# Kernel tuning notes

Measured on AMD Instinct MI355X. Metric: run time of the kernel, lower is better.

## Reference

```python
import jax, jax.numpy as jnp
import numpy as np

D_MODEL = 1024
N_HEADS = 16
D_Q = 64
D_V = 64
N_SEG = 16
EPS_LN = 1e-5
EPS_MEM = 1e-6


def setup_inputs() -> dict:
    key = jax.random.key(0)
    ks = jax.random.split(key, 10)
    N, T = 4, 4096
    inp = {
        "query_sequences": jax.random.normal(ks[0], (N, T, D_MODEL), dtype=jnp.float32),
        "key_sequences": jax.random.normal(ks[1], (N, T, D_MODEL), dtype=jnp.float32),
        "value_sequences": jax.random.normal(ks[2], (N, T, D_MODEL), dtype=jnp.float32),
        "Wq": jax.random.normal(ks[3], (D_MODEL, N_HEADS * D_Q), dtype=jnp.float32) * 0.02,
        "Wk": jax.random.normal(ks[4], (D_MODEL, N_HEADS * D_Q), dtype=jnp.float32) * 0.02,
        "Wv": jax.random.normal(ks[5], (D_MODEL, N_HEADS * D_V), dtype=jnp.float32) * 0.02,
        "Wo": jax.random.normal(ks[6], (N_HEADS * D_V, D_MODEL), dtype=jnp.float32) * 0.02,
        "ln_w": jnp.ones((D_MODEL,), dtype=jnp.float32),
        "ln_b": jnp.zeros((D_MODEL,), dtype=jnp.float32),
        "beta": jnp.ones((1,), dtype=jnp.float32),
    }
    return inp


def _layer_norm(x, w, b):
    mu = jnp.mean(x, axis=-1, keepdims=True)
    var = jnp.var(x, axis=-1, keepdims=True)
    return (x - mu) * jax.lax.rsqrt(var + EPS_LN) * w + b


def reference(query_sequences, key_sequences, value_sequences, Wq, Wk, Wv, Wo, ln_w, ln_b, beta):
    N, t, _ = query_sequences.shape
    S = t // N_SEG  # segment length (256)

    # qkv_norm applied to q, and (self-attention) to k and v as well
    qn = _layer_norm(query_sequences, ln_w, ln_b)
    kn = _layer_norm(key_sequences, ln_w, ln_b)
    vn = _layer_norm(value_sequences, ln_w, ln_b)

    # project and split heads -> [N, H, t, d]
    qh = (qn @ Wq).reshape(N, t, N_HEADS, D_Q).transpose(0, 2, 1, 3)
    kh = (kn @ Wk).reshape(N, t, N_HEADS, D_Q).transpose(0, 2, 1, 3)
    vh = (vn @ Wv).reshape(N, t, N_HEADS, D_V).transpose(0, 2, 1, 3)

    # segment: [N_SEG, N, H, S, d] so lax.scan iterates segments sequentially
    seg = lambda x, d: x.reshape(N, N_HEADS, N_SEG, S, d).transpose(2, 0, 1, 3, 4)
    q_segs, k_segs, v_segs = seg(qh, D_Q), seg(kh, D_Q), seg(vh, D_V)

    b_gate = jax.nn.sigmoid(beta)[0]            # scalar mixing gate
    scale = 1.0 / np.sqrt(D_Q).astype(np.float32)
    causal = jnp.tril(jnp.ones((S, S), dtype=bool))

    def step(carry, xs):
        mem, z = carry                          # [N,H,Dq,Dv], [N,H,Dq]
        qs, ks_, vs = xs                        # [N,H,S,d]
        sq = jax.nn.elu(qs) + 1.0
        sk = jax.nn.elu(ks_) + 1.0
        # retrieve from compressive memory
        num = jnp.einsum('nhsd,nhde->nhse', sq, mem)
        den = jnp.einsum('nhsd,nhd->nhs', sq, z)[..., None] + EPS_MEM
        a_mem = num / den                       # [N,H,S,Dv]
        # local causal softmax attention within the segment
        scores = jnp.einsum('nhsd,nhtd->nhst', qs, ks_) * scale
        scores = jnp.where(causal, scores, -jnp.inf)
        probs = jax.nn.softmax(scores, axis=-1)
        attn = jnp.einsum('nhst,nhtd->nhsd', probs, vs)
        out = b_gate * a_mem + (1.0 - b_gate) * attn
        # linear memory update
        mem = mem + jnp.einsum('nhsd,nhse->nhde', sk, vs)
        z = z + sk.sum(axis=2)
        return (mem, z), out

    mem0 = jnp.zeros((N, N_HEADS, D_Q, D_V), dtype=query_sequences.dtype)
    z0 = jnp.zeros((N, N_HEADS, D_Q), dtype=query_sequences.dtype)
    _, outs = jax.lax.scan(step, (mem0, z0), (q_segs, k_segs, v_segs))

    # outs: [N_SEG, N, H, S, Dv] -> [N, t, H*Dv]
    seqs = outs.transpose(1, 0, 3, 2, 4).reshape(N, t, N_HEADS * D_V)
    return seqs @ Wo
```

## Files before the change

kernel.cpp:

```cpp
#include <hip/hip_runtime.h>
#include <stdint.h>
#include <math.h>


typedef __attribute__((ext_vector_type(8))) short bf16x8_t;
typedef __attribute__((ext_vector_type(4))) short short4_t;
typedef __attribute__((ext_vector_type(4))) float f32x4;

__device__ __forceinline__ float bf2f(short s){
  union { unsigned u; float f; } v; v.u = ((unsigned)(unsigned short)s) << 16; return v.f;
}
__device__ __forceinline__ short f2bf(float f){
  union { float fl; unsigned u; } v; v.fl = f;
  unsigned r = v.u + 0x7FFFu + ((v.u >> 16) & 1u);
  return (short)(unsigned short)(r >> 16);
}
__device__ __forceinline__ f32x4 mfma16(bf16x8_t a, bf16x8_t b, f32x4 c){
  return __builtin_amdgcn_mfma_f32_16x16x32_bf16(a, b, c, 0, 0, 0);
}
__device__ __forceinline__ void gl_lds16(const short* g, short* l){
  __builtin_amdgcn_global_load_lds((const __attribute__((address_space(1))) void*)g,
                                   (__attribute__((address_space(3))) void*)l, 16, 0, 0);
}

__global__ __launch_bounds__(256) void ln_kernel(const float* __restrict__ x,
                                                 const float* __restrict__ gw,
                                                 const float* __restrict__ gb,
                                                 short* __restrict__ out){
  const int row = blockIdx.x, tid = threadIdx.x;
  const float4 v = *reinterpret_cast<const float4*>(x + (size_t)row*1024 + tid*4);
  float s  = v.x + v.y + v.z + v.w;
  float s2 = v.x*v.x + v.y*v.y + v.z*v.z + v.w*v.w;
  #pragma unroll
  for (int off = 1; off < 64; off <<= 1){
    s  += __shfl_xor(s,  off);
    s2 += __shfl_xor(s2, off);
  }
  __shared__ float red[8];
  if ((tid & 63) == 0){ red[tid>>6] = s; red[4 + (tid>>6)] = s2; }
  __syncthreads();
  s  = red[0] + red[1] + red[2] + red[3];
  s2 = red[4] + red[5] + red[6] + red[7];
  const float mu  = s * (1.0f/1024.0f);
  const float var = s2 * (1.0f/1024.0f) - mu*mu;
  const float rs  = rsqrtf(var + 1e-5f);
  const float4 wv = *reinterpret_cast<const float4*>(gw + tid*4);
  const float4 bv = *reinterpret_cast<const float4*>(gb + tid*4);
  short4_t o;
  o[0] = f2bf((v.x-mu)*rs*wv.x + bv.x);
  o[1] = f2bf((v.y-mu)*rs*wv.y + bv.y);
  o[2] = f2bf((v.z-mu)*rs*wv.z + bv.z);
  o[3] = f2bf((v.w-mu)*rs*wv.w + bv.w);
  *reinterpret_cast<short4_t*>(out + (size_t)row*1024 + tid*4) = o;
}

__global__ __launch_bounds__(256) void wcast(const float* __restrict__ W, short* __restrict__ Wt){
  __shared__ float tile[64][65];
  const int bx = blockIdx.x, by = blockIdx.y, tid = threadIdx.x;
  #pragma unroll
  for (int p=0;p<4;++p){
    int idx = p*256 + tid;
    int r = idx >> 4, c4 = (idx & 15) << 2;
    const float4 v = *reinterpret_cast<const float4*>(W + (size_t)(by*64 + r)*1024 + bx*64 + c4);
    tile[r][c4+0] = v.x; tile[r][c4+1] = v.y; tile[r][c4+2] = v.z; tile[r][c4+3] = v.w;
  }
  __syncthreads();
  #pragma unroll
  for (int p=0;p<4;++p){
    int idx = p*256 + tid;
    int r = idx >> 4, c4 = (idx & 15) << 2;
    short4_t o;
    o[0] = f2bf(tile[c4+0][r]); o[1] = f2bf(tile[c4+1][r]);
    o[2] = f2bf(tile[c4+2][r]); o[3] = f2bf(tile[c4+3][r]);
    *reinterpret_cast<short4_t*>(Wt + (size_t)(bx*64 + r)*1024 + by*64 + c4) = o;
  }
}

__global__ __launch_bounds__(512, 2) void gemm256(const short* __restrict__ A, const short* __restrict__ Bt,
                                                  void* __restrict__ C, int mode){
  extern __shared__ short smem[];
  short* As = smem;
  short* Bs = smem + 32768;
  const int tid = threadIdx.x;
  const int m0 = blockIdx.x * 256;
  const int c0 = blockIdx.y * 256;
  const int lane = tid & 63, wid = tid >> 6;
  const int wr = wid >> 2, wc = wid & 3;
  const int l15 = lane & 15, lhi = lane >> 4;

  const short* Asrc[4]; const short* Bsrc[4];
  #pragma unroll
  for (int p=0;p<4;++p){
    int i = tid + 512*p;
    int r = i >> 3, g = (i & 7) ^ (r & 7);
    Asrc[p] = A  + (size_t)(m0 + r)*1024 + g*8;
    Bsrc[p] = Bt + (size_t)(c0 + r)*1024 + g*8;
  }

  f32x4 acc[8][4];
  #pragma unroll
  for (int m=0;m<8;++m)
    #pragma unroll
    for (int n=0;n<4;++n) acc[m][n] = (f32x4){0.f,0.f,0.f,0.f};

  #define STAGE_A(t) { short* _d=&As[((t)&1)<<14]; int _k=(t)<<6; \
      gl_lds16(Asrc[0]+_k, _d+tid*8); gl_lds16(Asrc[1]+_k, _d+4096+tid*8); \
      gl_lds16(Asrc[2]+_k, _d+8192+tid*8); gl_lds16(Asrc[3]+_k, _d+12288+tid*8); }
  #define STAGE_B(t) { short* _d=&Bs[((t)&1)<<14]; int _k=(t)<<6; \
      gl_lds16(Bsrc[0]+_k, _d+tid*8); gl_lds16(Bsrc[1]+_k, _d+4096+tid*8); \
      gl_lds16(Bsrc[2]+_k, _d+8192+tid*8); gl_lds16(Bsrc[3]+_k, _d+12288+tid*8); }

  STAGE_A(0); STAGE_B(0);
  asm volatile("s_waitcnt vmcnt(0)" ::: "memory");
  __builtin_amdgcn_s_barrier();

  for (int t = 0; t < 16; ++t){
    const short* Ab = &As[(t & 1) << 14];
    const short* Bb = &Bs[(t & 1) << 14];
    if (t < 15){ STAGE_A(t+1); STAGE_B(t+1); }
    bf16x8_t af[4][2], bfr[4][2];
    #pragma unroll
    for (int m=0;m<4;++m){
      int r = wr*128 + m*16 + l15;
      #pragma unroll
      for (int ks=0;ks<2;++ks){
        int sl = (ks*4 + lhi) ^ (r & 7);
        af[m][ks] = *reinterpret_cast<const bf16x8_t*>(&Ab[r*64 + sl*8]);
      }
    }
    #pragma unroll
    for (int n=0;n<2;++n){
      int r = wc*64 + n*16 + l15;
      #pragma unroll
      for (int ks=0;ks<2;++ks){
        int sl = (ks*4 + lhi) ^ (r & 7);
        bfr[n][ks] = *reinterpret_cast<const bf16x8_t*>(&Bb[r*64 + sl*8]);
      }
    }
    __builtin_amdgcn_s_setprio(1);
    #pragma unroll
    for (int m=0;m<4;++m)
      #pragma unroll
      for (int n=0;n<2;++n)
        #pragma unroll
        for (int ks=0;ks<2;++ks)
          acc[m][n] = mfma16(af[m][ks], bfr[n][ks], acc[m][n]);
    __builtin_amdgcn_s_setprio(0);
    #pragma unroll
    for (int n=2;n<4;++n){
      int r = wc*64 + n*16 + l15;
      #pragma unroll
      for (int ks=0;ks<2;++ks){
        int sl = (ks*4 + lhi) ^ (r & 7);
        bfr[n][ks] = *reinterpret_cast<const bf16x8_t*>(&Bb[r*64 + sl*8]);
      }
    }
    __builtin_amdgcn_s_setprio(1);
    #pragma unroll
    for (int m=0;m<4;++m)
      #pragma unroll
      for (int n=2;n<4;++n)
        #pragma unroll
        for (int ks=0;ks<2;++ks)
          acc[m][n] = mfma16(af[m][ks], bfr[n][ks], acc[m][n]);
    __builtin_amdgcn_s_setprio(0);
    #pragma unroll
    for (int m=0;m<4;++m){
      int r = wr*128 + 64 + m*16 + l15;
      #pragma unroll
      for (int ks=0;ks<2;++ks){
        int sl = (ks*4 + lhi) ^ (r & 7);
        af[m][ks] = *reinterpret_cast<const bf16x8_t*>(&Ab[r*64 + sl*8]);
      }
    }
    __builtin_amdgcn_s_setprio(1);
    #pragma unroll
    for (int m=0;m<4;++m)
      #pragma unroll
      for (int n=0;n<2;++n)
        #pragma unroll
        for (int ks=0;ks<2;++ks)
          acc[4+m][n] = mfma16(af[m][ks], bfr[n][ks], acc[4+m][n]);
    __builtin_amdgcn_s_setprio(0);
    __builtin_amdgcn_s_setprio(1);
    #pragma unroll
    for (int m=0;m<4;++m)
      #pragma unroll
      for (int n=2;n<4;++n)
        #pragma unroll
        for (int ks=0;ks<2;++ks)
          acc[4+m][n] = mfma16(af[m][ks], bfr[n][ks], acc[4+m][n]);
    __builtin_amdgcn_s_setprio(0);
    asm volatile("s_waitcnt vmcnt(0)" ::: "memory");
    __builtin_amdgcn_s_barrier();
  }
  #undef STAGE_A
  #undef STAGE_B

  if (mode == 0){
    short* Cb = (short*)C;
    #pragma unroll
    for (int m=0;m<8;++m)
      #pragma unroll
      for (int n=0;n<4;++n)
        #pragma unroll
        for (int j=0;j<4;++j){
          int row = m0 + wr*128 + m*16 + lhi*4 + j;
          int col = c0 + wc*64 + n*16 + l15;
          size_t oidx = ((size_t)((row>>12)*16 + (col>>6)) * 4096 + (size_t)(row & 4095)) * 64 + (col & 63);
          Cb[oidx] = f2bf(acc[m][n][j]);
        }
  } else if (mode == 2){
    short* Cb = (short*)C;
    #pragma unroll
    for (int m=0;m<8;++m)
      #pragma unroll
      for (int n=0;n<4;++n){
        int rowb = m0 + wr*128 + m*16 + lhi*4;
        int col  = c0 + wc*64 + n*16 + l15;
        int nh = ((rowb>>12)<<4) + (col>>6);
        int e  = col & 63;
        int tt = rowb & 4095;
        short4_t o;
        #pragma unroll
        for (int j=0;j<4;++j) o[j] = f2bf(acc[m][n][j]);
        *reinterpret_cast<short4_t*>(&Cb[((size_t)nh*64 + e)*4096 + tt]) = o;
      }
  } else {
    float* Cf = (float*)C;
    #pragma unroll
    for (int m=0;m<8;++m)
      #pragma unroll
      for (int n=0;n<4;++n)
        #pragma unroll
        for (int j=0;j<4;++j){
          int row = m0 + wr*128 + m*16 + lhi*4 + j;
          int col = c0 + wc*64 + n*16 + l15;
          Cf[(size_t)row*1024 + col] = acc[m][n][j];
        }
  }
}

__global__ __launch_bounds__(256) void stageA(const short* __restrict__ kh, const short* __restrict__ vhT,
                                              short* __restrict__ delta_b, float* __restrict__ zd){
  const int seg = blockIdx.x, nh = blockIdx.y, tid = threadIdx.x;
  const int lane = tid & 63, w = tid >> 6;
  const int l15 = lane & 15, lhi = lane >> 4;
  __shared__ short skT[64*256];
  const size_t thead = (size_t)nh*4096 + (size_t)seg*256;

  #pragma unroll
  for (int ch=0; ch<8; ++ch){
    int s  = ch*32 + (tid>>3);
    int lc = (tid&7)*8;
    bf16x8_t kv = *reinterpret_cast<const bf16x8_t*>(kh + (thead + s)*64 + lc);
    #pragma unroll
    for (int j=0;j<8;++j){
      float f = bf2f(kv[j]);
      short sv = f2bf((f > 0.f) ? (f + 1.f) : __expf(f));
      int d = lc + j;
      int bo = ((d*256 + s) << 1) ^ (((d>>3)&7) << 4);
      *reinterpret_cast<short*>(reinterpret_cast<char*>(skT) + bo) = sv;
    }
  }
  __syncthreads();

  bf16x8_t ones;
  #pragma unroll
  for (int i=0;i<8;++i) ones[i] = (short)0x3F80;

  f32x4 dacc[4], zacc[4];
  #pragma unroll
  for (int jf=0;jf<4;++jf){ dacc[jf] = (f32x4){0.f,0.f,0.f,0.f}; zacc[jf] = (f32x4){0.f,0.f,0.f,0.f}; }

  #pragma unroll
  for (int ks=0; ks<8; ++ks){
    bf16x8_t av = *reinterpret_cast<const bf16x8_t*>(
        vhT + ((size_t)nh*64 + w*16 + l15)*4096 + (size_t)seg*256 + ks*32 + lhi*8);
    #pragma unroll
    for (int jf=0;jf<4;++jf){
      int d  = jf*16 + l15;
      int so = ks*32 + lhi*8;
      int bo = ((d*256 + so) << 1) ^ (((d>>3)&7) << 4);
      bf16x8_t bk = *reinterpret_cast<const bf16x8_t*>(reinterpret_cast<char*>(skT) + bo);
      dacc[jf] = mfma16(av, bk, dacc[jf]);
      if (w == 0) zacc[jf] = mfma16(ones, bk, zacc[jf]);
    }
  }

  short* dp = delta_b + (size_t)(seg*64 + nh)*4096;
  #pragma unroll
  for (int jf=0;jf<4;++jf)
    #pragma unroll
    for (int j=0;j<4;++j)
      dp[(w*16 + lhi*4 + j)*64 + jf*16 + l15] = f2bf(dacc[jf][j]);
  if (w == 0 && lhi == 0){
    #pragma unroll
    for (int jf=0;jf<4;++jf)
      zd[(size_t)(seg*64 + nh)*64 + jf*16 + l15] = zacc[jf][0];
  }
}

__global__ __launch_bounds__(256) void stageB(const short* __restrict__ delta_b, const float* __restrict__ zd,
                                              short* __restrict__ mpre_b, float* __restrict__ zpre){
  const int c = blockIdx.x, nh = blockIdx.y, tid = threadIdx.x;
  const int idx = c*256 + tid;
  float acc = 0.f;
  for (int seg=0; seg<16; ++seg){
    size_t b = (size_t)(seg*64 + nh)*4096 + idx;
    mpre_b[b] = f2bf(acc);
    acc += bf2f(delta_b[b]);
  }
  if (c == 0 && tid < 64){
    float za = 0.f;
    for (int seg=0; seg<16; ++seg){
      size_t zb = (size_t)(seg*64 + nh)*64 + tid;
      zpre[zb] = za;
      za += zd[zb];
    }
  }
}

__global__ __launch_bounds__(256, 3) void stageC(const short* __restrict__ qh, const short* __restrict__ kh,
    const short* __restrict__ vhT, const short* __restrict__ mpre_b, const float* __restrict__ z_pre,
    const float* __restrict__ beta, short* __restrict__ seqs)
{
  const int half = blockIdx.x;
  const int seg  = blockIdx.y;
  const int nh   = blockIdx.z;
  const int tid = threadIdx.x;
  const int lane = tid & 63, w = tid >> 6;
  const int l15 = lane & 15, lhi = lane >> 4;

  __shared__ float zl[64];
  __shared__ short pl[4][32][72];

  const size_t thead = (size_t)nh*4096 + (size_t)seg*256;

  if (tid < 64) zl[tid] = z_pre[(size_t)(seg*64 + nh)*64 + tid];
  __syncthreads();

  const float bg = 1.f / (1.f + __expf(-beta[0]));
  const float scale = 0.125f;
  bf16x8_t ones;
  #pragma unroll
  for (int i=0;i<8;++i) ones[i] = (short)0x3F80;

  const int tile = 2*w + (half ? (1 - (w & 1)) : (w & 1));
  const int nkt  = (tile >> 1) + 1;
  const int rb   = tile * 32;

  bf16x8_t aq[2][2];
  #pragma unroll
  for (int m=0;m<2;++m)
    #pragma unroll
    for (int ks=0;ks<2;++ks)
      aq[m][ks] = *reinterpret_cast<const bf16x8_t*>(qh + (thead + rb + m*16 + l15)*64 + ks*32 + lhi*8);

  f32x4 o_acc[2][4], l_acc[2];
  #pragma unroll
  for (int m=0;m<2;++m){
    l_acc[m] = (f32x4){0.f,0.f,0.f,0.f};
    #pragma unroll
    for (int jf=0;jf<4;++jf) o_acc[m][jf] = (f32x4){0.f,0.f,0.f,0.f};
  }

  for (int kt = 0; kt < nkt; ++kt){
    f32x4 s_acc[2][4];
    #pragma unroll
    for (int m=0;m<2;++m)
      #pragma unroll
      for (int jf=0;jf<4;++jf) s_acc[m][jf] = (f32x4){0.f,0.f,0.f,0.f};
    #pragma unroll
    for (int ks=0;ks<2;++ks){
      bf16x8_t bk[4];
      #pragma unroll
      for (int jf=0;jf<4;++jf)
        bk[jf] = *reinterpret_cast<const bf16x8_t*>(kh + (thead + kt*64 + jf*16 + l15)*64 + ks*32 + lhi*8);
      #pragma unroll
      for (int m=0;m<2;++m)
        #pragma unroll
        for (int jf=0;jf<4;++jf)
          s_acc[m][jf] = mfma16(aq[m][ks], bk[jf], s_acc[m][jf]);
    }
    const bool lastkt = (kt == nkt - 1);
    #pragma unroll
    for (int m=0;m<2;++m)
      #pragma unroll
      for (int jf=0;jf<4;++jf)
        #pragma unroll
        for (int j=0;j<4;++j){
          float vv = s_acc[m][jf][j] * scale;
          if (lastkt){
            int sr = rb + m*16 + lhi*4 + j;
            int tc = kt*64 + jf*16 + l15;
            if (tc > sr) vv = -INFINITY;
          }
          float pv = __expf(vv);
          pl[w][m*16 + lhi*4 + j][jf*16 + l15] = f2bf(pv);
        }
    #pragma unroll
    for (int ks2=0;ks2<2;++ks2){
      bf16x8_t ap[2], bv[4];
      #pragma unroll
      for (int m=0;m<2;++m)
        ap[m] = *reinterpret_cast<const bf16x8_t*>(&pl[w][m*16 + l15][ks2*32 + lhi*8]);
      #pragma unroll
      for (int jf=0;jf<4;++jf)
        bv[jf] = *reinterpret_cast<const bf16x8_t*>(
            vhT + ((size_t)nh*64 + jf*16 + l15)*4096 + (size_t)seg*256 + kt*64 + ks2*32 + lhi*8);
      #pragma unroll
      for (int m=0;m<2;++m){
        l_acc[m] = mfma16(ap[m], ones, l_acc[m]);
        #pragma unroll
        for (int jf=0;jf<4;++jf)
          o_acc[m][jf] = mfma16(ap[m], bv[jf], o_acc[m][jf]);
      }
    }
  }

  bf16x8_t sq[2][2];
  #pragma unroll
  for (int m=0;m<2;++m)
    #pragma unroll
    for (int ks=0;ks<2;++ks)
      #pragma unroll
      for (int i=0;i<8;++i){
        float f = bf2f(aq[m][ks][i]);
        sq[m][ks][i] = f2bf((f > 0.f) ? (f + 1.f) : __expf(f));
      }
  bf16x8_t bz[2];
  #pragma unroll
  for (int ks=0;ks<2;++ks)
    #pragma unroll
    for (int i=0;i<8;++i) bz[ks][i] = f2bf(zl[ks*32 + lhi*8 + i]);

  const short* mpbase = mpre_b + (size_t)(seg*64 + nh)*4096;
  f32x4 n_acc[2][4], d_acc[2];
  #pragma unroll
  for (int m=0;m<2;++m){
    d_acc[m] = (f32x4){0.f,0.f,0.f,0.f};
    #pragma unroll
    for (int jf=0;jf<4;++jf) n_acc[m][jf] = (f32x4){0.f,0.f,0.f,0.f};
  }
  #pragma unroll
  for (int ks=0;ks<2;++ks){
    bf16x8_t bm[4];
    #pragma unroll
    for (int jf=0;jf<4;++jf)
      bm[jf] = *reinterpret_cast<const bf16x8_t*>(mpbase + (jf*16 + l15)*64 + ks*32 + lhi*8);
    #pragma unroll
    for (int m=0;m<2;++m){
      #pragma unroll
      for (int jf=0;jf<4;++jf) n_acc[m][jf] = mfma16(sq[m][ks], bm[jf], n_acc[m][jf]);
      d_acc[m] = mfma16(sq[m][ks], bz[ks], d_acc[m]);
    }
  }

  const int nb = nh >> 4, hh = nh & 15;
  #pragma unroll
  for (int m=0;m<2;++m)
    #pragma unroll
    for (int jf=0;jf<4;++jf)
      #pragma unroll
      for (int j=0;j<4;++j){
        float attn = o_acc[m][jf][j] / l_acc[m][j];
        float amem = n_acc[m][jf][j] / (d_acc[m][j] + 1e-6f);
        float ov = bg*amem + (1.f-bg)*attn;
        int srow = rb + m*16 + lhi*4 + j;
        seqs[((size_t)nb*4096 + (size_t)seg*256 + srow)*1024 + hh*64 + jf*16 + l15] = f2bf(ov);
      }
}

extern "C" void kernel_launch(void* const* d_in, const int* in_sizes, int n_in,
                              void* d_out, int out_size, void* d_ws, size_t ws_size,
                              hipStream_t stream){
  (void)in_sizes; (void)n_in; (void)out_size; (void)ws_size;
  const float* q    = (const float*)d_in[0];
  const float* k    = (const float*)d_in[1];
  const float* v    = (const float*)d_in[2];
  const float* Wq   = (const float*)d_in[3];
  const float* Wk   = (const float*)d_in[4];
  const float* Wv   = (const float*)d_in[5];
  const float* Wo   = (const float*)d_in[6];
  const float* lnw  = (const float*)d_in[7];
  const float* lnb  = (const float*)d_in[8];
  const float* beta = (const float*)d_in[9];
  char* ws = (char*)d_ws;
  const size_t MB = 1024ull*1024ull;
  short* WqT    = (short*)(ws + 0*MB);
  short* WkT    = (short*)(ws + 2*MB);
  short* WvT    = (short*)(ws + 4*MB);
  short* WoT    = (short*)(ws + 6*MB);
  short* xn     = (short*)(ws + 8*MB);
  short* seqs   = xn;
  short* qh     = (short*)(ws + 40*MB);
  short* kh     = (short*)(ws + 72*MB);
  short* vhT    = (short*)(ws + 104*MB);
  short* delta_b= (short*)(ws + 136*MB);
  float* zd     = (float*)(ws + 144*MB);
  short* mpre_b = (short*)(ws + 145*MB);
  float* zpre   = (float*)(ws + 153*MB);

  dim3 tg(16,16);
  wcast<<<tg,256,0,stream>>>(Wq, WqT);
  wcast<<<tg,256,0,stream>>>(Wk, WkT);
  wcast<<<tg,256,0,stream>>>(Wv, WvT);
  wcast<<<tg,256,0,stream>>>(Wo, WoT);

  dim3 gg(64,4);
  const size_t lds_gemm = 131072;
  ln_kernel<<<16384,256,0,stream>>>(q, lnw, lnb, xn);
  gemm256<<<gg,512,lds_gemm,stream>>>(xn, WqT, (void*)qh, 0);
  ln_kernel<<<16384,256,0,stream>>>(k, lnw, lnb, xn);
  gemm256<<<gg,512,lds_gemm,stream>>>(xn, WkT, (void*)kh, 0);
  ln_kernel<<<16384,256,0,stream>>>(v, lnw, lnb, xn);
  gemm256<<<gg,512,lds_gemm,stream>>>(xn, WvT, (void*)vhT, 2);

  stageA<<<dim3(16,64),256,0,stream>>>(kh, vhT, delta_b, zd);
  stageB<<<dim3(16,64),256,0,stream>>>(delta_b, zd, mpre_b, zpre);
  stageC<<<dim3(2,16,64),256,0,stream>>>(qh, kh, vhT, mpre_b, zpre, beta, seqs);
  gemm256<<<gg,512,lds_gemm,stream>>>(seqs, WoT, d_out, 1);
}
```

Baseline: 321.5 us.

## Batch LN, weight-cast and QKV GEMM launches; fold stageC halves into one block

Merges the four weight-cast launches into one 3D grid and the three layernorm launches into one, using the output buffer as scratch for the q/k normalized activations. The three QKV projection GEMMs become a single launch with a z-dimension, giving 768 blocks instead of three serial 256-block launches. The goal is to cut launch overhead and the tail idle time of each under-filled GEMM wave. stageC now has each block handle both causal halves in a loop, with V loads hoisted ahead of the score MFMAs; this halves the block count and lengthens each block's work.

```diff
diff --git a/kernel.cpp b/kernel.cpp
--- a/kernel.cpp
+++ b/kernel.cpp
@@ -23,11 +23,14 @@
                                    (__attribute__((address_space(3))) void*)l, 16, 0, 0);
 }
 
-__global__ __launch_bounds__(256) void ln_kernel(const float* __restrict__ x,
-                                                 const float* __restrict__ gw,
-                                                 const float* __restrict__ gb,
-                                                 short* __restrict__ out){
-  const int row = blockIdx.x, tid = threadIdx.x;
+__global__ __launch_bounds__(256) void ln3(const float* __restrict__ xq, const float* __restrict__ xk,
+                                           const float* __restrict__ xv,
+                                           const float* __restrict__ gw, const float* __restrict__ gb,
+                                           short* __restrict__ oq, short* __restrict__ ok,
+                                           short* __restrict__ ov){
+  const int row = blockIdx.x, which = blockIdx.y, tid = threadIdx.x;
+  const float* x = which == 0 ? xq : which == 1 ? xk : xv;
+  short* out     = which == 0 ? oq : which == 1 ? ok : ov;
   const float4 v = *reinterpret_cast<const float4*>(x + (size_t)row*1024 + tid*4);
   float s  = v.x + v.y + v.z + v.w;
   float s2 = v.x*v.x + v.y*v.y + v.z*v.z + v.w*v.w;
@@ -54,7 +57,13 @@
   *reinterpret_cast<short4_t*>(out + (size_t)row*1024 + tid*4) = o;
 }
 
-__global__ __launch_bounds__(256) void wcast(const float* __restrict__ W, short* __restrict__ Wt){
+__global__ __launch_bounds__(256) void wcast4(const float* __restrict__ W0, const float* __restrict__ W1,
+                                              const float* __restrict__ W2, const float* __restrict__ W3,
+                                              short* __restrict__ T0, short* __restrict__ T1,
+                                              short* __restrict__ T2, short* __restrict__ T3){
+  const int z = blockIdx.z;
+  const float* W = z == 0 ? W0 : z == 1 ? W1 : z == 2 ? W2 : W3;
+  short* Wt      = z == 0 ? T0 : z == 1 ? T1 : z == 2 ? T2 : T3;
   __shared__ float tile[64][65];
   const int bx = blockIdx.x, by = blockIdx.y, tid = threadIdx.x;
   #pragma unroll
@@ -76,9 +85,8 @@
   }
 }
 
-__global__ __launch_bounds__(512, 2) void gemm256(const short* __restrict__ A, const short* __restrict__ Bt,
-                                                  void* __restrict__ C, int mode){
-  extern __shared__ short smem[];
+__device__ __forceinline__ void gemm_body(short* smem, const short* __restrict__ A,
+                                          const short* __restrict__ Bt, void* __restrict__ C, int mode){
   short* As = smem;
   short* Bs = smem + 32768;
   const int tid = threadIdx.x;
@@ -239,6 +247,23 @@
           Cf[(size_t)row*1024 + col] = acc[m][n][j];
         }
   }
+}
+
+__global__ __launch_bounds__(512, 2) void gemm_qkv(const short* __restrict__ A0, const short* __restrict__ A1,
+    const short* __restrict__ A2, const short* __restrict__ B0, const short* __restrict__ B1,
+    const short* __restrict__ B2, short* __restrict__ C0, short* __restrict__ C1, short* __restrict__ C2){
+  extern __shared__ short smem[];
+  const int z = blockIdx.z;
+  const short* A = z == 0 ? A0 : z == 1 ? A1 : A2;
+  const short* B = z == 0 ? B0 : z == 1 ? B1 : B2;
+  short* C       = z == 0 ? C0 : z == 1 ? C1 : C2;
+  gemm_body(smem, A, B, (void*)C, z == 2 ? 2 : 0);
+}
+
+__global__ __launch_bounds__(512, 2) void gemm_wo(const short* __restrict__ A, const short* __restrict__ Bt,
+                                                  float* __restrict__ C){
+  extern __shared__ short smem[];
+  gemm_body(smem, A, Bt, (void*)C, 1);
 }
 
 __global__ __launch_bounds__(256) void stageA(const short* __restrict__ kh, const short* __restrict__ vhT,
@@ -325,9 +350,8 @@
     const short* __restrict__ vhT, const short* __restrict__ mpre_b, const float* __restrict__ z_pre,
     const float* __restrict__ beta, short* __restrict__ seqs)
 {
-  const int half = blockIdx.x;
-  const int seg  = blockIdx.y;
-  const int nh   = blockIdx.z;
+  const int seg  = blockIdx.x;
+  const int nh   = blockIdx.y;
   const int tid = threadIdx.x;
   const int lane = tid & 63, w = tid >> 6;
   const int l15 = lane & 15, lhi = lane >> 4;
@@ -345,131 +369,137 @@
   bf16x8_t ones;
   #pragma unroll
   for (int i=0;i<8;++i) ones[i] = (short)0x3F80;
-
-  const int tile = 2*w + (half ? (1 - (w & 1)) : (w & 1));
-  const int nkt  = (tile >> 1) + 1;
-  const int rb   = tile * 32;
-
-  bf16x8_t aq[2][2];
-  #pragma unroll
-  for (int m=0;m<2;++m)
+  const short* mpbase = mpre_b + (size_t)(seg*64 + nh)*4096;
+  const int nb = nh >> 4, hh = nh & 15;
+
+  for (int p = 0; p < 2; ++p){
+    const int tile = p ? (7 - w) : w;
+    const int nkt  = (tile >> 1) + 1;
+    const int rb   = tile * 32;
+
+    bf16x8_t aq[2][2];
+    #pragma unroll
+    for (int m=0;m<2;++m)
+      #pragma unroll
+      for (int ks=0;ks<2;++ks)
+        aq[m][ks] = *reinterpret_cast<const bf16x8_t*>(qh + (thead + rb + m*16 + l15)*64 + ks*32 + lhi*8);
+
+    f32x4 o_acc[2][4], l_acc[2];
+    #pragma unroll
+    for (int m=0;m<2;++m){
+      l_acc[m] = (f32x4){0.f,0.f,0.f,0.f};
+      #pragma unroll
+      for (int jf=0;jf<4;++jf) o_acc[m][jf] = (f32x4){0.f,0.f,0.f,0.f};
+    }
+
+    for (int kt = 0; kt < nkt; ++kt){
+      bf16x8_t bv[4][2];
+      #pragma unroll
+      for (int jf=0;jf<4;++jf)
+        #pragma unroll
+        for (int ks2=0;ks2<2;++ks2)
+          bv[jf][ks2] = *reinterpret_cast<const bf16x8_t*>(
+              vhT + ((size_t)nh*64 + jf*16 + l15)*4096 + (size_t)seg*256 + kt*64 + ks2*32 + lhi*8);
+
+      f32x4 s_acc[2][4];
+      #pragma unroll
+      for (int m=0;m<2;++m)
+        #pragma unroll
+        for (int jf=0;jf<4;++jf) s_acc[m][jf] = (f32x4){0.f,0.f,0.f,0.f};
+      #pragma unroll
+      for (int ks=0;ks<2;++ks){
+        bf16x8_t bk[4];
+        #pragma unroll
+        for (int jf=0;jf<4;++jf)
+          bk[jf] = *reinterpret_cast<const bf16x8_t*>(kh + (thead + kt*64 + jf*16 + l15)*64 + ks*32 + lhi*8);
+        #pragma unroll
+        for (int m=0;m<2;++m)
+          #pragma unroll
+          for (int jf=0;jf<4;++jf)
+            s_acc[m][jf] = mfma16(aq[m][ks], bk[jf], s_acc[m][jf]);
+      }
+      const bool lastkt = (kt == nkt - 1);
+      #pragma unroll
+      for (int m=0;m<2;++m)
+        #pragma unroll
+        for (int jf=0;jf<4;++jf)
+          #pragma unroll
+          for (int j=0;j<4;++j){
+            float vv = s_acc[m][jf][j] * scale;
+            if (lastkt){
+              int sr = rb + m*16 + lhi*4 + j;
+              int tc = kt*64 + jf*16 + l15;
+              if (tc > sr) vv = -INFINITY;
+            }
+            float pv = __expf(vv);
+            pl[w][m*16 + lhi*4 + j][jf*16 + l15] = f2bf(pv);
+          }
+      #pragma unroll
+      for (int ks2=0;ks2<2;++ks2){
+        bf16x8_t ap[2];
+        #pragma unroll
+        for (int m=0;m<2;++m)
+          ap[m] = *reinterpret_cast<const bf16x8_t*>(&pl[w][m*16 + l15][ks2*32 + lhi*8]);
+        #pragma unroll
+        for (int m=0;m<2;++m){
+          l_acc[m] = mfma16(ap[m], ones, l_acc[m]);
+          #pragma unroll
+          for (int jf=0;jf<4;++jf)
+            o_acc[m][jf] = mfma16(ap[m], bv[jf][ks2], o_acc[m][jf]);
+        }
+      }
+    }
+
+    bf16x8_t sq[2][2];
+    #pragma unroll
+    for (int m=0;m<2;++m)
+      #pragma unroll
+      for (int ks=0;ks<2;++ks)
+        #pragma unroll
+        for (int i=0;i<8;++i){
+          float f = bf2f(aq[m][ks][i]);
+          sq[m][ks][i] = f2bf((f > 0.f) ? (f + 1.f) : __expf(f));
+        }
+    bf16x8_t bz[2];
     #pragma unroll
     for (int ks=0;ks<2;++ks)
-      aq[m][ks] = *reinterpret_cast<const bf16x8_t*>(qh + (thead + rb + m*16 + l15)*64 + ks*32 + lhi*8);
-
-  f32x4 o_acc[2][4], l_acc[2];
-  #pragma unroll
-  for (int m=0;m<2;++m){
-    l_acc[m] = (f32x4){0.f,0.f,0.f,0.f};
-    #pragma unroll
-    for (int jf=0;jf<4;++jf) o_acc[m][jf] = (f32x4){0.f,0.f,0.f,0.f};
-  }
-
-  for (int kt = 0; kt < nkt; ++kt){
-    f32x4 s_acc[2][4];
+      #pragma unroll
+      for (int i=0;i<8;++i) bz[ks][i] = f2bf(zl[ks*32 + lhi*8 + i]);
+
+    f32x4 n_acc[2][4], d_acc[2];
+    #pragma unroll
+    for (int m=0;m<2;++m){
+      d_acc[m] = (f32x4){0.f,0.f,0.f,0.f};
+      #pragma unroll
+      for (int jf=0;jf<4;++jf) n_acc[m][jf] = (f32x4){0.f,0.f,0.f,0.f};
+    }
+    #pragma unroll
+    for (int ks=0;ks<2;++ks){
+      bf16x8_t bm[4];
+      #pragma unroll
+      for (int jf=0;jf<4;++jf)
+        bm[jf] = *reinterpret_cast<const bf16x8_t*>(mpbase + (jf*16 + l15)*64 + ks*32 + lhi*8);
+      #pragma unroll
+      for (int m=0;m<2;++m){
+        #pragma unroll
+        for (int jf=0;jf<4;++jf) n_acc[m][jf] = mfma16(sq[m][ks], bm[jf], n_acc[m][jf]);
+        d_acc[m] = mfma16(sq[m][ks], bz[ks], d_acc[m]);
+      }
+    }
+
     #pragma unroll
     for (int m=0;m<2;++m)
       #pragma unroll
-      for (int jf=0;jf<4;++jf) s_acc[m][jf] = (f32x4){0.f,0.f,0.f,0.f};
-    #pragma unroll
-    for (int ks=0;ks<2;++ks){
-      bf16x8_t bk[4];
-      #pragma unroll
       for (int jf=0;jf<4;++jf)
-        bk[jf] = *reinterpret_cast<const bf16x8_t*>(kh + (thead + kt*64 + jf*16 + l15)*64 + ks*32 + lhi*8);
-      #pragma unroll
-      for (int m=0;m<2;++m)
-        #pragma unroll
-        for (int jf=0;jf<4;++jf)
-          s_acc[m][jf] = mfma16(aq[m][ks], bk[jf], s_acc[m][jf]);
-    }
-    const bool lastkt = (kt == nkt - 1);
-    #pragma unroll
-    for (int m=0;m<2;++m)
-      #pragma unroll
-      for (int jf=0;jf<4;++jf)
         #pragma unroll
         for (int j=0;j<4;++j){
-          float vv = s_acc[m][jf][j] * scale;
-          if (lastkt){
-            int sr = rb + m*16 + lhi*4 + j;
-            int tc = kt*64 + jf*16 + l15;
-            if (tc > sr) vv = -INFINITY;
-          }
-          float pv = __expf(vv);
-          pl[w][m*16 + lhi*4 + j][jf*16 + l15] = f2bf(pv);
+          float attn = o_acc[m][jf][j] / l_acc[m][j];
+          float amem = n_acc[m][jf][j] / (d_acc[m][j] + 1e-6f);
+          float ov = bg*amem + (1.f-bg)*attn;
+          int srow = rb + m*16 + lhi*4 + j;
+          seqs[((size_t)nb*4096 + (size_t)seg*256 + srow)*1024 + hh*64 + jf*16 + l15] = f2bf(ov);
         }
-    #pragma unroll
-    for (int ks2=0;ks2<2;++ks2){
-      bf16x8_t ap[2], bv[4];
-      #pragma unroll
-      for (int m=0;m<2;++m)
-        ap[m] = *reinterpret_cast<const bf16x8_t*>(&pl[w][m*16 + l15][ks2*32 + lhi*8]);
-      #pragma unroll
-      for (int jf=0;jf<4;++jf)
-        bv[jf] = *reinterpret_cast<const bf16x8_t*>(
-            vhT + ((size_t)nh*64 + jf*16 + l15)*4096 + (size_t)seg*256 + kt*64 + ks2*32 + lhi*8);
-      #pragma unroll
-      for (int m=0;m<2;++m){
-        l_acc[m] = mfma16(ap[m], ones, l_acc[m]);
-        #pragma unroll
-        for (int jf=0;jf<4;++jf)
-          o_acc[m][jf] = mfma16(ap[m], bv[jf], o_acc[m][jf]);
-      }
-    }
-  }
-
-  bf16x8_t sq[2][2];
-  #pragma unroll
-  for (int m=0;m<2;++m)
-    #pragma unroll
-    for (int ks=0;ks<2;++ks)
-      #pragma unroll
-      for (int i=0;i<8;++i){
-        float f = bf2f(aq[m][ks][i]);
-        sq[m][ks][i] = f2bf((f > 0.f) ? (f + 1.f) : __expf(f));
-      }
-  bf16x8_t bz[2];
-  #pragma unroll
-  for (int ks=0;ks<2;++ks)
-    #pragma unroll
-    for (int i=0;i<8;++i) bz[ks][i] = f2bf(zl[ks*32 + lhi*8 + i]);
-
-  const short* mpbase = mpre_b + (size_t)(seg*64 + nh)*4096;
-  f32x4 n_acc[2][4], d_acc[2];
-  #pragma unroll
-  for (int m=0;m<2;++m){
-    d_acc[m] = (f32x4){0.f,0.f,0.f,0.f};
-    #pragma unroll
-    for (int jf=0;jf<4;++jf) n_acc[m][jf] = (f32x4){0.f,0.f,0.f,0.f};
-  }
-  #pragma unroll
-  for (int ks=0;ks<2;++ks){
-    bf16x8_t bm[4];
-    #pragma unroll
-    for (int jf=0;jf<4;++jf)
-      bm[jf] = *reinterpret_cast<const bf16x8_t*>(mpbase + (jf*16 + l15)*64 + ks*32 + lhi*8);
-    #pragma unroll
-    for (int m=0;m<2;++m){
-      #pragma unroll
-      for (int jf=0;jf<4;++jf) n_acc[m][jf] = mfma16(sq[m][ks], bm[jf], n_acc[m][jf]);
-      d_acc[m] = mfma16(sq[m][ks], bz[ks], d_acc[m]);
-    }
-  }
-
-  const int nb = nh >> 4, hh = nh & 15;
-  #pragma unroll
-  for (int m=0;m<2;++m)
-    #pragma unroll
-    for (int jf=0;jf<4;++jf)
-      #pragma unroll
-      for (int j=0;j<4;++j){
-        float attn = o_acc[m][jf][j] / l_acc[m][j];
-        float amem = n_acc[m][jf][j] / (d_acc[m][j] + 1e-6f);
-        float ov = bg*amem + (1.f-bg)*attn;
-        int srow = rb + m*16 + lhi*4 + j;
-        seqs[((size_t)nb*4096 + (size_t)seg*256 + srow)*1024 + hh*64 + jf*16 + l15] = f2bf(ov);
-      }
+  }
 }
 
 extern "C" void kernel_launch(void* const* d_in, const int* in_sizes, int n_in,
@@ -492,8 +522,8 @@
   short* WkT    = (short*)(ws + 2*MB);
   short* WvT    = (short*)(ws + 4*MB);
   short* WoT    = (short*)(ws + 6*MB);
-  short* xn     = (short*)(ws + 8*MB);
-  short* seqs   = xn;
+  short* xn_v   = (short*)(ws + 8*MB);
+  short* seqs   = xn_v;
   short* qh     = (short*)(ws + 40*MB);
   short* kh     = (short*)(ws + 72*MB);
   short* vhT    = (short*)(ws + 104*MB);
@@ -501,24 +531,17 @@
   float* zd     = (float*)(ws + 144*MB);
   short* mpre_b = (short*)(ws + 145*MB);
   float* zpre   = (float*)(ws + 153*MB);
-
-  dim3 tg(16,16);
-  wcast<<<tg,256,0,stream>>>(Wq, WqT);
-  wcast<<<tg,256,0,stream>>>(Wk, WkT);
-  wcast<<<tg,256,0,stream>>>(Wv, WvT);
-  wcast<<<tg,256,0,stream>>>(Wo, WoT);
-
-  dim3 gg(64,4);
+  short* xn_q   = (short*)d_out;
+  short* xn_k   = (short*)d_out + 16384ull*1024ull;
+
+  wcast4<<<dim3(16,16,4),256,0,stream>>>(Wq,Wk,Wv,Wo, WqT,WkT,WvT,WoT);
+  ln3<<<dim3(16384,3),256,0,stream>>>(q,k,v, lnw,lnb, xn_q,xn_k,xn_v);
+
   const size_t lds_gemm = 131072;
-  ln_kernel<<<16384,256,0,stream>>>(q, lnw, lnb, xn);
-  gemm256<<<gg,512,lds_gemm,stream>>>(xn, WqT, (void*)qh, 0);
-  ln_kernel<<<16384,256,0,stream>>>(k, lnw, lnb, xn);
-  gemm256<<<gg,512,lds_gemm,stream>>>(xn, WkT, (void*)kh, 0);
-  ln_kernel<<<16384,256,0,stream>>>(v, lnw, lnb, xn);
-  gemm256<<<gg,512,lds_gemm,stream>>>(xn, WvT, (void*)vhT, 2);
+  gemm_qkv<<<dim3(64,4,3),512,lds_gemm,stream>>>(xn_q,xn_k,xn_v, WqT,WkT,WvT, qh,kh,vhT);
 
   stageA<<<dim3(16,64),256,0,stream>>>(kh, vhT, delta_b, zd);
   stageB<<<dim3(16,64),256,0,stream>>>(delta_b, zd, mpre_b, zpre);
-  stageC<<<dim3(2,16,64),256,0,stream>>>(qh, kh, vhT, mpre_b, zpre, beta, seqs);
-  gemm256<<<gg,512,lds_gemm,stream>>>(seqs, WoT, d_out, 1);
-}
+  stageC<<<dim3(16,64),256,0,stream>>>(qh, kh, vhT, mpre_b, zpre, beta, seqs);
+  gemm_wo<<<dim3(64,4),512,lds_gemm,stream>>>(seqs, WoT, (float*)d_out);
+}
```

Result: no change. 315.3 us (-1.9%).
